# Optimization experiments

Measured on AMD Instinct MI355X. Metric: run time of the kernel, lower is better.

Reference implementation:

```python
import jax, jax.numpy as jnp
import numpy as np

EPS = 1e-08


def setup_inputs() -> dict:
    key = jax.random.key(0)
    k1, k2, k3 = jax.random.split(key, 3)
    B, C, D, H, W = 2, 4, 128, 192, 192
    net_output = jax.random.normal(k1, (B, C, D, H, W), dtype=jnp.float32)
    target = jax.random.randint(k2, (B, 1, D, H, W), 0, C, dtype=jnp.int64)
    dist = jax.random.uniform(k3, (B, D, H, W), dtype=jnp.float32)
    return {"net_output": net_output, "target": target, "dist": dist}


def reference(net_output, target, dist):
    # net_output: [B, C, D, H, W]; target: [B, 1, D, H, W] int; dist: [B, D, H, W]
    B, C = net_output.shape[0], net_output.shape[1]
    # one-hot scatter along channel dim (scatter_(1, target, 1))
    cls = jnp.arange(C, dtype=target.dtype).reshape((1, C) + (1,) * (net_output.ndim - 2))
    y_onehot = (target == cls).astype(net_output.dtype)  # [B, C, D, H, W]

    # channels i >= 1: overlay dist, then per-(b, i)-slice min-max normalize
    z = y_onehot[:, 1:] * dist[:, None]  # [B, C-1, D, H, W]
    spatial_axes = tuple(range(2, z.ndim))
    mn = jnp.min(z, axis=spatial_axes, keepdims=True)
    mx = jnp.max(z, axis=spatial_axes, keepdims=True)
    zn = (z - mn) / (mx + EPS - mn)
    dist_y = jnp.concatenate([y_onehot[:, :1], zn], axis=1)  # [B, C, D, H, W]
    dist_y = jax.lax.stop_gradient(dist_y)  # built under no_grad / from non-grad leaves

    # CrossEntropyLoss with soft (probability) targets: mean over batch+spatial
    logp = jax.nn.log_softmax(net_output, axis=1)
    loss = -(dist_y * logp).sum(axis=1).mean()
    return loss
```

## Files before the change

### kernel.cpp

```cpp
#include <hip/hip_runtime.h>

#define NB 2
#define NC 4
#define NS (128 * 192 * 192)
#define NTOT (NB * NS)
#define NSQ (NS / 4)
#define EPSF 1e-8f
#define INF_BITS 0x7F800000u

#define BLOCKS 4608
#define TPB 256
#define HALFB (BLOCKS / 2)
#define STRIDE (HALFB * TPB)


__global__ void k_fused(const float* __restrict__ x,
                        const int* __restrict__ tgt,
                        const float* __restrict__ dist,
                        float* __restrict__ part) {
    const int b = (blockIdx.x >= HALFB) ? 1 : 0;
    const int bid = blockIdx.x - b * HALFB;
    const int q0 = bid * TPB + threadIdx.x;
    const int q1 = q0 + STRIDE;

    const int4* t4 = (const int4*)tgt + (size_t)b * NSQ;
    const float4* d4 = (const float4*)dist + (size_t)b * NSQ;
    const float4* xb = (const float4*)x + (size_t)b * NC * NSQ;

    float4 ax0 = xb[q0];
    float4 ax1 = xb[q0 + NSQ];
    float4 ax2 = xb[q0 + 2 * NSQ];
    float4 ax3 = xb[q0 + 3 * NSQ];
    float4 bx0 = xb[q1];
    float4 bx1 = xb[q1 + NSQ];
    float4 bx2 = xb[q1 + 2 * NSQ];
    float4 bx3 = xb[q1 + 3 * NSQ];
    int4 at = t4[q0];
    int4 bt = t4[q1];
    float4 ad = d4[q0];
    float4 bd = d4[q1];

    float mn1 = __uint_as_float(INF_BITS), mn2 = mn1, mn3 = mn1;
    float mx1 = 0.f, mx2 = 0.f, mx3 = 0.f;
    float P1 = 0.f, P2 = 0.f, P3 = 0.f;
    float Q1 = 0.f, Q2 = 0.f, Q3 = 0.f;
    float R0 = 0.f;

    auto vox = [&](float a0, float a1, float a2, float a3, int tt, float dv) {
        float m = fmaxf(fmaxf(a0, a1), fmaxf(a2, a3));
        float e = __expf(a0 - m) + __expf(a1 - m) + __expf(a2 - m) + __expf(a3 - m);
        float lse = m + __logf(e);
        float z1 = (tt == 1) ? dv : 0.f;
        float z2 = (tt == 2) ? dv : 0.f;
        float z3 = (tt == 3) ? dv : 0.f;
        mn1 = fminf(mn1, z1); mx1 = fmaxf(mx1, z1);
        mn2 = fminf(mn2, z2); mx2 = fmaxf(mx2, z2);
        mn3 = fminf(mn3, z3); mx3 = fmaxf(mx3, z3);
        float l1 = a1 - lse, l2 = a2 - lse, l3 = a3 - lse;
        P1 += z1 * l1; P2 += z2 * l2; P3 += z3 * l3;
        Q1 += l1; Q2 += l2; Q3 += l3;
        R0 += (tt == 0) ? (a0 - lse) : 0.f;
    };

    vox(ax0.x, ax1.x, ax2.x, ax3.x, at.x, ad.x);
    vox(ax0.y, ax1.y, ax2.y, ax3.y, at.y, ad.y);
    vox(ax0.z, ax1.z, ax2.z, ax3.z, at.z, ad.z);
    vox(ax0.w, ax1.w, ax2.w, ax3.w, at.w, ad.w);
    vox(bx0.x, bx1.x, bx2.x, bx3.x, bt.x, bd.x);
    vox(bx0.y, bx1.y, bx2.y, bx3.y, bt.y, bd.y);
    vox(bx0.z, bx1.z, bx2.z, bx3.z, bt.z, bd.z);
    vox(bx0.w, bx1.w, bx2.w, bx3.w, bt.w, bd.w);

    for (int off = 32; off; off >>= 1) {
        mn1 = fminf(mn1, __shfl_down(mn1, off, 64));
        mn2 = fminf(mn2, __shfl_down(mn2, off, 64));
        mn3 = fminf(mn3, __shfl_down(mn3, off, 64));
        mx1 = fmaxf(mx1, __shfl_down(mx1, off, 64));
        mx2 = fmaxf(mx2, __shfl_down(mx2, off, 64));
        mx3 = fmaxf(mx3, __shfl_down(mx3, off, 64));
        P1 += __shfl_down(P1, off, 64);
        P2 += __shfl_down(P2, off, 64);
        P3 += __shfl_down(P3, off, 64);
        Q1 += __shfl_down(Q1, off, 64);
        Q2 += __shfl_down(Q2, off, 64);
        Q3 += __shfl_down(Q3, off, 64);
        R0 += __shfl_down(R0, off, 64);
    }

    __shared__ float sv[4][13];
    const int wid = threadIdx.x >> 6;
    if ((threadIdx.x & 63) == 0) {
        sv[wid][0] = mn1; sv[wid][1] = mn2; sv[wid][2] = mn3;
        sv[wid][3] = mx1; sv[wid][4] = mx2; sv[wid][5] = mx3;
        sv[wid][6] = P1;  sv[wid][7] = P2;  sv[wid][8] = P3;
        sv[wid][9] = Q1;  sv[wid][10] = Q2; sv[wid][11] = Q3;
        sv[wid][12] = R0;
    }
    __syncthreads();
    const int i = threadIdx.x;
    if (i < 13) {
        float v = sv[0][i];
        if (i < 3)      v = fminf(fminf(v, sv[1][i]), fminf(sv[2][i], sv[3][i]));
        else if (i < 6) v = fmaxf(fmaxf(v, sv[1][i]), fmaxf(sv[2][i], sv[3][i]));
        else            v = v + sv[1][i] + sv[2][i] + sv[3][i];
        part[(size_t)blockIdx.x * 16 + i] = v;
    }
}

__global__ __launch_bounds__(256, 1)
void k_final(const float* __restrict__ part, float* __restrict__ out) {
    const int t = threadIdx.x;
    const int batch = t >> 7;
    const int lane7 = t & 127;

    float mn[3] = {__uint_as_float(INF_BITS), __uint_as_float(INF_BITS), __uint_as_float(INF_BITS)};
    float mx[3] = {0.f, 0.f, 0.f};
    double P[3] = {0, 0, 0}, Q[3] = {0, 0, 0}, R0 = 0;

    for (int k = 0; k < HALFB / 128; k++) {
        const float4* r = (const float4*)(part + (size_t)(batch * HALFB + k * 128 + lane7) * 16);
        float4 r0 = r[0];
        float4 r1 = r[1];
        float4 r2 = r[2];
        float4 r3 = r[3];
        mn[0] = fminf(mn[0], r0.x); mn[1] = fminf(mn[1], r0.y); mn[2] = fminf(mn[2], r0.z);
        mx[0] = fmaxf(mx[0], r0.w); mx[1] = fmaxf(mx[1], r1.x); mx[2] = fmaxf(mx[2], r1.y);
        P[0] += (double)r1.z; P[1] += (double)r1.w; P[2] += (double)r2.x;
        Q[0] += (double)r2.y; Q[1] += (double)r2.z; Q[2] += (double)r2.w;
        R0 += (double)r3.x;
    }

    for (int off = 32; off; off >>= 1) {
#pragma unroll
        for (int j = 0; j < 3; j++) {
            mn[j] = fminf(mn[j], __shfl_down(mn[j], off, 64));
            mx[j] = fmaxf(mx[j], __shfl_down(mx[j], off, 64));
            P[j] += __shfl_down(P[j], off, 64);
            Q[j] += __shfl_down(Q[j], off, 64);
        }
        R0 += __shfl_down(R0, off, 64);
    }

    __shared__ float smn[4][3], smx[4][3];
    __shared__ double sP[4][3], sQ[4][3], sR[4];
    const int wid = t >> 6;
    if ((t & 63) == 0) {
#pragma unroll
        for (int j = 0; j < 3; j++) {
            smn[wid][j] = mn[j]; smx[wid][j] = mx[j];
            sP[wid][j] = P[j];   sQ[wid][j] = Q[j];
        }
        sR[wid] = R0;
    }
    __syncthreads();
    if (t == 0) {
        double acc = 0.0;
#pragma unroll
        for (int b = 0; b < 2; b++) {
            const int w0 = 2 * b, w1 = 2 * b + 1;
            acc += sR[w0] + sR[w1];
#pragma unroll
            for (int j = 0; j < 3; j++) {
                float mnf = fminf(smn[w0][j], smn[w1][j]);
                float mxf = fmaxf(smx[w0][j], smx[w1][j]);
                float sf = 1.0f / (mxf + EPSF - mnf);
                acc += (double)sf * ((sP[w0][j] + sP[w1][j]) - (double)mnf * (sQ[w0][j] + sQ[w1][j]));
            }
        }
        out[0] = (float)(-acc / (double)NTOT);
    }
}

extern "C" void kernel_launch(void* const* d_in, const int* in_sizes, int n_in,
                              void* d_out, int out_size, void* d_ws, size_t ws_size,
                              hipStream_t stream) {
    const float* net = (const float*)d_in[0];
    const int* tgt = (const int*)d_in[1];
    const float* dist = (const float*)d_in[2];
    float* part = (float*)d_ws;

    k_fused<<<BLOCKS, TPB, 0, stream>>>(net, tgt, dist, part);
    k_final<<<1, 256, 0, stream>>>(part, (float*)d_out);
}
```

Before: 270.3 us.

## Stream inputs through double-buffered LDS via async global_load_lds with fewer blocks

```diff
diff --git a/kernel.cpp b/kernel.cpp
--- a/kernel.cpp
+++ b/kernel.cpp
@@ -1,50 +1,61 @@
 #include <hip/hip_runtime.h>
+#include <stdint.h>
 
 #define NB 2
-#define NC 4
 #define NS (128 * 192 * 192)
 #define NTOT (NB * NS)
 #define NSQ (NS / 4)
 #define EPSF 1e-8f
 #define INF_BITS 0x7F800000u
 
-#define BLOCKS 4608
 #define TPB 256
-#define HALFB (BLOCKS / 2)
-#define STRIDE (HALFB * TPB)
-
-
-__global__ void k_fused(const float* __restrict__ x,
-                        const int* __restrict__ tgt,
-                        const float* __restrict__ dist,
-                        float* __restrict__ part) {
-    const int b = (blockIdx.x >= HALFB) ? 1 : 0;
-    const int bid = blockIdx.x - b * HALFB;
-    const int q0 = bid * TPB + threadIdx.x;
-    const int q1 = q0 + STRIDE;
-
-    const int4* t4 = (const int4*)tgt + (size_t)b * NSQ;
+#define BPB 1152
+#define BLOCKS (2 * BPB)
+#define STRIDE (BPB * TPB)
+#define ITERS (NSQ / STRIDE)
+
+
+typedef __attribute__((address_space(3))) void lds_vp;
+typedef const __attribute__((address_space(1))) void glb_vp;
+
+__device__ __forceinline__ void dma16(void* lds_base, const void* gptr) {
+    __builtin_amdgcn_global_load_lds((glb_vp*)gptr, (lds_vp*)lds_base, 16, 0, 0);
+}
+
+__global__ __launch_bounds__(TPB)
+void k_fused(const float* __restrict__ x,
+             const int* __restrict__ tgt,
+             const float* __restrict__ dist,
+             float* __restrict__ part) {
+    __shared__ float4 sx[2][4][TPB];
+    __shared__ int4   st[2][TPB];
+    __shared__ float4 sd[2][TPB];
+
+    const int b = (blockIdx.x >= BPB) ? 1 : 0;
+    const int bid = blockIdx.x - b * BPB;
+    const int tid = threadIdx.x;
+    const int wb = (tid >> 6) << 6;
+    const int q0 = bid * TPB + tid;
+
+    const float4* xb = (const float4*)x + (size_t)b * 4 * NSQ;
+    const int4*   t4 = (const int4*)tgt + (size_t)b * NSQ;
     const float4* d4 = (const float4*)dist + (size_t)b * NSQ;
-    const float4* xb = (const float4*)x + (size_t)b * NC * NSQ;
-
-    float4 ax0 = xb[q0];
-    float4 ax1 = xb[q0 + NSQ];
-    float4 ax2 = xb[q0 + 2 * NSQ];
-    float4 ax3 = xb[q0 + 3 * NSQ];
-    float4 bx0 = xb[q1];
-    float4 bx1 = xb[q1 + NSQ];
-    float4 bx2 = xb[q1 + 2 * NSQ];
-    float4 bx3 = xb[q1 + 3 * NSQ];
-    int4 at = t4[q0];
-    int4 bt = t4[q1];
-    float4 ad = d4[q0];
-    float4 bd = d4[q1];
 
     float mn1 = __uint_as_float(INF_BITS), mn2 = mn1, mn3 = mn1;
     float mx1 = 0.f, mx2 = 0.f, mx3 = 0.f;
     float P1 = 0.f, P2 = 0.f, P3 = 0.f;
     float Q1 = 0.f, Q2 = 0.f, Q3 = 0.f;
     float R0 = 0.f;
+
+    auto issue = [&](int p, int i) {
+        const int q = q0 + i * STRIDE;
+        dma16(&sx[p][0][wb], &xb[q]);
+        dma16(&sx[p][1][wb], &xb[q + NSQ]);
+        dma16(&sx[p][2][wb], &xb[q + 2 * NSQ]);
+        dma16(&sx[p][3][wb], &xb[q + 3 * NSQ]);
+        dma16(&st[p][wb], &t4[q]);
+        dma16(&sd[p][wb], &d4[q]);
+    };
 
     auto vox = [&](float a0, float a1, float a2, float a3, int tt, float dv) {
         float m = fmaxf(fmaxf(a0, a1), fmaxf(a2, a3));
@@ -62,14 +73,24 @@
         R0 += (tt == 0) ? (a0 - lse) : 0.f;
     };
 
-    vox(ax0.x, ax1.x, ax2.x, ax3.x, at.x, ad.x);
-    vox(ax0.y, ax1.y, ax2.y, ax3.y, at.y, ad.y);
-    vox(ax0.z, ax1.z, ax2.z, ax3.z, at.z, ad.z);
-    vox(ax0.w, ax1.w, ax2.w, ax3.w, at.w, ad.w);
-    vox(bx0.x, bx1.x, bx2.x, bx3.x, bt.x, bd.x);
-    vox(bx0.y, bx1.y, bx2.y, bx3.y, bt.y, bd.y);
-    vox(bx0.z, bx1.z, bx2.z, bx3.z, bt.z, bd.z);
-    vox(bx0.w, bx1.w, bx2.w, bx3.w, bt.w, bd.w);
+    issue(0, 0);
+#pragma unroll
+    for (int i = 0; i < ITERS; i++) {
+        const int p = i & 1;
+        asm volatile("s_waitcnt vmcnt(0)" ::: "memory");
+        float4 x0 = sx[p][0][tid];
+        float4 x1 = sx[p][1][tid];
+        float4 x2 = sx[p][2][tid];
+        float4 x3 = sx[p][3][tid];
+        int4   t  = st[p][tid];
+        float4 d  = sd[p][tid];
+        asm volatile("s_waitcnt lgkmcnt(0)" ::: "memory");
+        if (i + 1 < ITERS) issue(p ^ 1, i + 1);
+        vox(x0.x, x1.x, x2.x, x3.x, t.x, d.x);
+        vox(x0.y, x1.y, x2.y, x3.y, t.y, d.y);
+        vox(x0.z, x1.z, x2.z, x3.z, t.z, d.z);
+        vox(x0.w, x1.w, x2.w, x3.w, t.w, d.w);
+    }
 
     for (int off = 32; off; off >>= 1) {
         mn1 = fminf(mn1, __shfl_down(mn1, off, 64));
@@ -88,8 +109,8 @@
     }
 
     __shared__ float sv[4][13];
-    const int wid = threadIdx.x >> 6;
-    if ((threadIdx.x & 63) == 0) {
+    const int wid = tid >> 6;
+    if ((tid & 63) == 0) {
         sv[wid][0] = mn1; sv[wid][1] = mn2; sv[wid][2] = mn3;
         sv[wid][3] = mx1; sv[wid][4] = mx2; sv[wid][5] = mx3;
         sv[wid][6] = P1;  sv[wid][7] = P2;  sv[wid][8] = P3;
@@ -97,13 +118,12 @@
         sv[wid][12] = R0;
     }
     __syncthreads();
-    const int i = threadIdx.x;
-    if (i < 13) {
-        float v = sv[0][i];
-        if (i < 3)      v = fminf(fminf(v, sv[1][i]), fminf(sv[2][i], sv[3][i]));
-        else if (i < 6) v = fmaxf(fmaxf(v, sv[1][i]), fmaxf(sv[2][i], sv[3][i]));
-        else            v = v + sv[1][i] + sv[2][i] + sv[3][i];
-        part[(size_t)blockIdx.x * 16 + i] = v;
+    if (tid < 13) {
+        float v = sv[0][tid];
+        if (tid < 3)      v = fminf(fminf(v, sv[1][tid]), fminf(sv[2][tid], sv[3][tid]));
+        else if (tid < 6) v = fmaxf(fmaxf(v, sv[1][tid]), fmaxf(sv[2][tid], sv[3][tid]));
+        else              v = v + sv[1][tid] + sv[2][tid] + sv[3][tid];
+        part[(size_t)blockIdx.x * 16 + tid] = v;
     }
 }
 
@@ -117,8 +137,9 @@
     float mx[3] = {0.f, 0.f, 0.f};
     double P[3] = {0, 0, 0}, Q[3] = {0, 0, 0}, R0 = 0;
 
-    for (int k = 0; k < HALFB / 128; k++) {
-        const float4* r = (const float4*)(part + (size_t)(batch * HALFB + k * 128 + lane7) * 16);
+#pragma unroll
+    for (int k = 0; k < BPB / 128; k++) {
+        const float4* r = (const float4*)(part + (size_t)(batch * BPB + k * 128 + lane7) * 16);
         float4 r0 = r[0];
         float4 r1 = r[1];
         float4 r2 = r[2];
```

Measured after the change: 266.9 us. No clear change (-1.3%).
